# Performance work log

Measured on AMD Instinct MI355X. Metric: run time of the kernel, lower is better.

## Reference

```python
import jax, jax.numpy as jnp
import numpy as np

T, H, F, E = 1024, 2048, 4096, 8


def setup_inputs() -> dict:
    key = jax.random.key(0)
    ks = jax.random.split(key, 5)
    s = 0.02
    return {
        "x": jax.random.normal(ks[0], (1, 1, T, H), dtype=jnp.float32),
        "w_gate": jax.random.normal(ks[1], (H, E), dtype=jnp.float32) * s,
        "w1": jax.random.normal(ks[2], (E, H, F), dtype=jnp.float32) * s,
        "w3": jax.random.normal(ks[3], (E, H, F), dtype=jnp.float32) * s,
        "w2": jax.random.normal(ks[4], (E, F, H), dtype=jnp.float32) * s,
    }


def _top2_weights(logits):
    # Faithful to top_2(): emulated top-2 via max/eq/mask, then 2-way softmax
    # w0 = 1/(1+exp(ex1-ex0)) for the top-1 expert, 1-w0 for the top-2 expert.
    neg_min = jnp.finfo(logits.dtype).min
    ex0 = jnp.max(logits, axis=-1, keepdims=True)            # (1,1,T,1)
    cond0 = (logits == ex0)                                   # top-1 indicator (1,1,T,E)
    masked = jnp.where(cond0, neg_min, logits)
    ex1 = jnp.max(masked, axis=-1, keepdims=True)            # second max
    cond1 = (masked == ex1)                                   # top-2 indicator
    w0 = 1.0 / (1.0 + jnp.exp(ex1 - ex0))                    # sigmoid(ex0-ex1)
    c0 = cond0.astype(logits.dtype)
    c1 = cond1.astype(logits.dtype)
    # c0*w0 - c1*(w0-1) == c0*w0 + c1*(1-w0)
    return c0 * w0 - c1 * (w0 - 1.0)                         # (1,1,T,E)


def reference(x, w_gate, w1, w3, w2):
    # x: (1,1,T,H)
    logits = jnp.einsum("abth,he->abte", x, w_gate)          # gate (1,1,T,E)
    weights = _top2_weights(logits)                           # (1,1,T,E)
    # SwiGLU experts, all experts on all tokens (dense, as in per-device replica)
    h1 = jnp.einsum("abth,ehf->eabtf", x, w1)
    h3 = jnp.einsum("abth,ehf->eabtf", x, w3)
    y = jnp.einsum("eabtf,efh->eabth", jax.nn.silu(h1) * h3, w2)
    # per-expert scale then sum over experts (= all-gather + reduce-mask matmul)
    out = jnp.einsum("eabth,abte->abth", y, weights)
    return out
```

## Files before the change

kernel.cpp:

```cpp
#include <hip/hip_runtime.h>
#include <hip/hip_bf16.h>

#define T_DIM 1024
#define H_DIM 2048
#define F_DIM 4096
#define E_DIM 8

typedef unsigned short u16;
typedef unsigned int u32;
typedef __attribute__((ext_vector_type(8))) short bf16x8;
typedef __attribute__((ext_vector_type(4))) float f32x4;

__device__ __forceinline__ u16 f2bf(float f) {
  u32 u = __builtin_bit_cast(u32, f);
  u32 r = (u + 0x7fffu + ((u >> 16) & 1u)) >> 16;
  return (u16)r;
}

__global__ __launch_bounds__(256) void gate_cvt_kernel(
    const float* __restrict__ x, const float* __restrict__ wg,
    u16* __restrict__ xb, float* __restrict__ wts) {
  int wave = threadIdx.x >> 6;
  int lane = threadIdx.x & 63;
  int t = blockIdx.x * 4 + wave;
  const float4* x4 = reinterpret_cast<const float4*>(x) + (size_t)t * 512;
  ushort4* xb4 = reinterpret_cast<ushort4*>(xb) + (size_t)t * 512;
  const float4* wg4 = reinterpret_cast<const float4*>(wg);

  float acc[8];
#pragma unroll
  for (int e = 0; e < 8; e++) acc[e] = 0.f;

#pragma unroll
  for (int i = 0; i < 8; i++) {
    int idx = i * 64 + lane;
    float4 v = x4[idx];
    ushort4 o = {f2bf(v.x), f2bf(v.y), f2bf(v.z), f2bf(v.w)};
    xb4[idx] = o;
    float xs[4] = {v.x, v.y, v.z, v.w};
    int hbase = idx * 4;
#pragma unroll
    for (int j = 0; j < 4; j++) {
      float4 wa = wg4[(hbase + j) * 2];
      float4 wb = wg4[(hbase + j) * 2 + 1];
      acc[0] += xs[j] * wa.x; acc[1] += xs[j] * wa.y;
      acc[2] += xs[j] * wa.z; acc[3] += xs[j] * wa.w;
      acc[4] += xs[j] * wb.x; acc[5] += xs[j] * wb.y;
      acc[6] += xs[j] * wb.z; acc[7] += xs[j] * wb.w;
    }
  }
#pragma unroll
  for (int e = 0; e < 8; e++) {
#pragma unroll
    for (int off = 32; off > 0; off >>= 1) acc[e] += __shfl_xor(acc[e], off, 64);
  }
  if (lane == 0) {
    const float NEG_MIN = -3.402823466e38f;
    float ex0 = acc[0];
#pragma unroll
    for (int e = 1; e < 8; e++) ex0 = fmaxf(ex0, acc[e]);
    float masked[8];
#pragma unroll
    for (int e = 0; e < 8; e++) masked[e] = (acc[e] == ex0) ? NEG_MIN : acc[e];
    float ex1 = masked[0];
#pragma unroll
    for (int e = 1; e < 8; e++) ex1 = fmaxf(ex1, masked[e]);
    float w0 = 1.f / (1.f + expf(ex1 - ex0));
#pragma unroll
    for (int e = 0; e < 8; e++) {
      float w = (acc[e] == ex0) ? w0 : ((masked[e] == ex1) ? (1.f - w0) : 0.f);
      wts[t * 8 + e] = w;
    }
  }
}

__global__ __launch_bounds__(512) void route_kernel(
    const float* __restrict__ wts, int* __restrict__ tlist,
    int* __restrict__ counts) {
  int e = threadIdx.x >> 6;
  int lane = threadIdx.x & 63;
  int base = 0;
  for (int c = 0; c < T_DIM; c += 64) {
    float w = wts[(c + lane) * 8 + e];
    unsigned long long m = __ballot(w != 0.f);
    if (w != 0.f) {
      int pos = base + __popcll(m & ((1ull << lane) - 1ull));
      tlist[e * T_DIM + pos] = c + lane;
    }
    base += __popcll(m);
  }
  if (lane == 0) counts[e] = base;
}

__global__ __launch_bounds__(256, 2) void h_kernel(
    const u16* __restrict__ xb, const float* __restrict__ w1,
    const float* __restrict__ w3, u16* __restrict__ hout,
    const int* __restrict__ tlist, const int* __restrict__ counts) {
  int el = blockIdx.z;
  int ne = counts[el];
  int t0 = blockIdx.y * 128;
  if (t0 >= ne) return;

  __shared__ u16 As[128 * 72];
  __shared__ u16 B1s[64 * 72];
  __shared__ u16 B3s[64 * 72];
  __shared__ int toks[128];

  int f0 = blockIdx.x * 64;
  const float* b1 = w1 + (long)el * H_DIM * F_DIM;
  const float* b3 = w3 + (long)el * H_DIM * F_DIM;
  int tid = threadIdx.x;
  if (tid < 128) {
    int i = t0 + tid;
    toks[tid] = tlist[el * T_DIM + (i < ne ? i : ne - 1)];
  }
  __syncthreads();

  int wave = tid >> 6, lane = tid & 63;
  int wm = wave >> 1, wn = wave & 1;
  int mrow = lane & 15, quad = lane >> 4;

  const u16* aptr[4];
  int aoff[4];
#pragma unroll
  for (int it = 0; it < 4; it++) {
    int chunk = tid + it * 256;
    int r = chunk >> 3, c8 = (chunk & 7) << 3;
    aptr[it] = xb + (long)toks[r] * H_DIM + c8;
    aoff[it] = r * 72 + c8;
  }

  int bf4 = (tid & 15) << 2;
  int bk0 = (tid >> 4) << 2;
  int bwoff[4];
#pragma unroll
  for (int j = 0; j < 4; j++) {
    int f = bf4 + j;
    bwoff[j] = f * 72 + (bk0 ^ (((f >> 2) & 7) << 3));
  }
  const float* gb1 = b1 + (long)bk0 * F_DIM + f0 + bf4;
  const float* gb3 = b3 + (long)bk0 * F_DIM + f0 + bf4;

  int aroff[4][2], broff[2][2];
#pragma unroll
  for (int mt = 0; mt < 4; mt++)
#pragma unroll
    for (int kh = 0; kh < 2; kh++)
      aroff[mt][kh] = (wm * 64 + mt * 16 + mrow) * 72 + kh * 32 + quad * 8;
#pragma unroll
  for (int nt = 0; nt < 2; nt++) {
    int row = wn * 32 + nt * 16 + mrow;
    int sw = ((row >> 2) & 7) << 3;
#pragma unroll
    for (int kh = 0; kh < 2; kh++)
      broff[nt][kh] = row * 72 + ((kh * 32 + quad * 8) ^ sw);
  }

  f32x4 acc1[4][2], acc3[4][2];
#pragma unroll
  for (int mt = 0; mt < 4; mt++)
#pragma unroll
    for (int nt = 0; nt < 2; nt++) { acc1[mt][nt] = (f32x4)(0.f); acc3[mt][nt] = (f32x4)(0.f); }

  for (int kt = 0; kt < H_DIM; kt += 64) {
#pragma unroll
    for (int it = 0; it < 4; it++) {
      uint4 v = *reinterpret_cast<const uint4*>(aptr[it] + kt);
      *reinterpret_cast<uint4*>(&As[aoff[it]]) = v;
    }
    float4 r1[4], r3[4];
    const float* g1 = gb1 + (long)kt * F_DIM;
    const float* g3 = gb3 + (long)kt * F_DIM;
#pragma unroll
    for (int kk = 0; kk < 4; kk++) {
      r1[kk] = *reinterpret_cast<const float4*>(g1 + (long)kk * F_DIM);
      r3[kk] = *reinterpret_cast<const float4*>(g3 + (long)kk * F_DIM);
    }
#pragma unroll
    for (int j = 0; j < 4; j++) {
      u32 lo1 = (u32)f2bf(((const float*)&r1[0])[j]) | ((u32)f2bf(((const float*)&r1[1])[j]) << 16);
      u32 hi1 = (u32)f2bf(((const float*)&r1[2])[j]) | ((u32)f2bf(((const float*)&r1[3])[j]) << 16);
      u32 lo3 = (u32)f2bf(((const float*)&r3[0])[j]) | ((u32)f2bf(((const float*)&r3[1])[j]) << 16);
      u32 hi3 = (u32)f2bf(((const float*)&r3[2])[j]) | ((u32)f2bf(((const float*)&r3[3])[j]) << 16);
      uint2 p1 = {lo1, hi1}, p3 = {lo3, hi3};
      *reinterpret_cast<uint2*>(&B1s[bwoff[j]]) = p1;
      *reinterpret_cast<uint2*>(&B3s[bwoff[j]]) = p3;
    }
    __syncthreads();
#pragma unroll
    for (int kh = 0; kh < 2; kh++) {
      bf16x8 af[4], b1f[2], b3f[2];
#pragma unroll
      for (int mt = 0; mt < 4; mt++)
        af[mt] = *reinterpret_cast<const bf16x8*>(&As[aroff[mt][kh]]);
#pragma unroll
      for (int nt = 0; nt < 2; nt++) {
        b1f[nt] = *reinterpret_cast<const bf16x8*>(&B1s[broff[nt][kh]]);
        b3f[nt] = *reinterpret_cast<const bf16x8*>(&B3s[broff[nt][kh]]);
      }
#pragma unroll
      for (int mt = 0; mt < 4; mt++)
#pragma unroll
        for (int nt = 0; nt < 2; nt++) {
          acc1[mt][nt] = __builtin_amdgcn_mfma_f32_16x16x32_bf16(af[mt], b1f[nt], acc1[mt][nt], 0, 0, 0);
          acc3[mt][nt] = __builtin_amdgcn_mfma_f32_16x16x32_bf16(af[mt], b3f[nt], acc3[mt][nt], 0, 0, 0);
        }
    }
    __syncthreads();
  }
  u16* hp = hout + (long)el * T_DIM * F_DIM;
#pragma unroll
  for (int mt = 0; mt < 4; mt++) {
#pragma unroll
    for (int r = 0; r < 4; r++) {
      int row = t0 + wm * 64 + mt * 16 + quad * 4 + r;
      if (row < ne) {
#pragma unroll
        for (int nt = 0; nt < 2; nt++) {
          int col = f0 + wn * 32 + nt * 16 + mrow;
          float v1 = acc1[mt][nt][r];
          float v3 = acc3[mt][nt][r];
          float sw = (v1 / (1.f + expf(-v1))) * v3;
          hp[(long)row * F_DIM + col] = f2bf(sw);
        }
      }
    }
  }
}

__global__ __launch_bounds__(256, 2) void y_kernel(
    const u16* __restrict__ h, const float* __restrict__ w2,
    const float* __restrict__ wts, float* __restrict__ out,
    const int* __restrict__ tlist, const int* __restrict__ counts) {
  int el = blockIdx.z;
  int ne = counts[el];
  int t0 = blockIdx.y * 128;
  if (t0 >= ne) return;

  __shared__ u16 As[128 * 72];
  __shared__ u16 Bs[64 * 72];
  int n0 = blockIdx.x * 64;
  const u16* a = h + (long)el * T_DIM * F_DIM;
  const float* b = w2 + (long)el * F_DIM * H_DIM;
  int tid = threadIdx.x;
  int wave = tid >> 6, lane = tid & 63;
  int wm = wave >> 1, wn = wave & 1;
  int mrow = lane & 15, quad = lane >> 4;

  int bh4 = (tid & 15) << 2;
  int bk0 = (tid >> 4) << 2;
  int bwoff[4];
#pragma unroll
  for (int j = 0; j < 4; j++) {
    int f = bh4 + j;
    bwoff[j] = f * 72 + (bk0 ^ (((f >> 2) & 7) << 3));
  }
  const float* gb = b + (long)bk0 * H_DIM + n0 + bh4;

  int aroff[4][2], broff[2][2];
#pragma unroll
  for (int mt = 0; mt < 4; mt++)
#pragma unroll
    for (int kh = 0; kh < 2; kh++)
      aroff[mt][kh] = (wm * 64 + mt * 16 + mrow) * 72 + kh * 32 + quad * 8;
#pragma unroll
  for (int nt = 0; nt < 2; nt++) {
    int row = wn * 32 + nt * 16 + mrow;
    int sw = ((row >> 2) & 7) << 3;
#pragma unroll
    for (int kh = 0; kh < 2; kh++)
      broff[nt][kh] = row * 72 + ((kh * 32 + quad * 8) ^ sw);
  }

  f32x4 acc[4][2];
#pragma unroll
  for (int mt = 0; mt < 4; mt++)
#pragma unroll
    for (int nt = 0; nt < 2; nt++) acc[mt][nt] = (f32x4)(0.f);

  for (int kt = 0; kt < F_DIM; kt += 64) {
#pragma unroll
    for (int it = 0; it < 4; it++) {
      int chunk = tid + it * 256;
      int r = chunk >> 3, c8 = (chunk & 7) << 3;
      uint4 v = *reinterpret_cast<const uint4*>(a + (long)(t0 + r) * F_DIM + kt + c8);
      *reinterpret_cast<uint4*>(&As[r * 72 + c8]) = v;
    }
    float4 rb[4];
    const float* g = gb + (long)kt * H_DIM;
#pragma unroll
    for (int kk = 0; kk < 4; kk++)
      rb[kk] = *reinterpret_cast<const float4*>(g + (long)kk * H_DIM);
#pragma unroll
    for (int j = 0; j < 4; j++) {
      u32 lo = (u32)f2bf(((const float*)&rb[0])[j]) | ((u32)f2bf(((const float*)&rb[1])[j]) << 16);
      u32 hi = (u32)f2bf(((const float*)&rb[2])[j]) | ((u32)f2bf(((const float*)&rb[3])[j]) << 16);
      uint2 pb = {lo, hi};
      *reinterpret_cast<uint2*>(&Bs[bwoff[j]]) = pb;
    }
    __syncthreads();
#pragma unroll
    for (int kh = 0; kh < 2; kh++) {
      bf16x8 af[4], bf[2];
#pragma unroll
      for (int mt = 0; mt < 4; mt++)
        af[mt] = *reinterpret_cast<const bf16x8*>(&As[aroff[mt][kh]]);
#pragma unroll
      for (int nt = 0; nt < 2; nt++)
        bf[nt] = *reinterpret_cast<const bf16x8*>(&Bs[broff[nt][kh]]);
#pragma unroll
      for (int mt = 0; mt < 4; mt++)
#pragma unroll
        for (int nt = 0; nt < 2; nt++)
          acc[mt][nt] = __builtin_amdgcn_mfma_f32_16x16x32_bf16(af[mt], bf[nt], acc[mt][nt], 0, 0, 0);
    }
    __syncthreads();
  }
#pragma unroll
  for (int mt = 0; mt < 4; mt++) {
#pragma unroll
    for (int r = 0; r < 4; r++) {
      int row = t0 + wm * 64 + mt * 16 + quad * 4 + r;
      if (row < ne) {
        int tok = tlist[el * T_DIM + row];
        float wt = wts[tok * 8 + el];
#pragma unroll
        for (int nt = 0; nt < 2; nt++) {
          int col = n0 + wn * 32 + nt * 16 + mrow;
          unsafeAtomicAdd(&out[(long)tok * H_DIM + col], acc[mt][nt][r] * wt);
        }
      }
    }
  }
}

extern "C" void kernel_launch(void* const* d_in, const int* in_sizes, int n_in,
                              void* d_out, int out_size, void* d_ws, size_t ws_size,
                              hipStream_t stream) {
  const float* x  = (const float*)d_in[0];
  const float* wg = (const float*)d_in[1];
  const float* w1 = (const float*)d_in[2];
  const float* w3 = (const float*)d_in[3];
  const float* w2 = (const float*)d_in[4];
  float* out = (float*)d_out;

  char* p = (char*)d_ws;
  u16* xb = (u16*)p;            p += (size_t)T_DIM * H_DIM * 2;
  float* wts = (float*)p;       p += (size_t)T_DIM * E_DIM * 4;
  int* tlist = (int*)p;         p += (size_t)E_DIM * T_DIM * 4;
  int* counts = (int*)p;        p += 256;
  u16* hbuf = (u16*)p;

  gate_cvt_kernel<<<T_DIM / 4, 256, 0, stream>>>(x, wg, xb, wts);
  route_kernel<<<1, 512, 0, stream>>>(wts, tlist, counts);
  hipMemsetAsync(d_out, 0, (size_t)out_size * 4, stream);

  h_kernel<<<dim3(F_DIM / 64, T_DIM / 128, E_DIM), 256, 0, stream>>>(
      xb, w1, w3, hbuf, tlist, counts);
  y_kernel<<<dim3(H_DIM / 64, T_DIM / 128, E_DIM), 256, 0, stream>>>(
      hbuf, w2, wts, out, tlist, counts);
}
```

Baseline: 900.9 us.

## Double-buffer activation tiles via direct global-to-LDS loads and prefetch weights

Both expert GEMM kernels now load the bf16 activation tile straight into a double-buffered LDS array with global_load_lds. The next K-tile's activations and fp32 weights are prefetched while the current tile is computed, with manual waitcnt and barriers in place of __syncthreads. The A tile drops its padded layout for an XOR swizzle, and launch bounds ask for 3 blocks per CU. The goal is to hide global-load latency behind the MFMA work. The cost is more LDS and register pressure, and the hand-written vmcnt/lgkmcnt sync is fragile.

```diff
diff --git a/kernel.cpp b/kernel.cpp
--- a/kernel.cpp
+++ b/kernel.cpp
@@ -15,6 +15,18 @@
   u32 u = __builtin_bit_cast(u32, f);
   u32 r = (u + 0x7fffu + ((u >> 16) & 1u)) >> 16;
   return (u16)r;
+}
+
+__device__ __forceinline__ void gld_lds16(const void* g, void* l) {
+  __builtin_amdgcn_global_load_lds(
+      (const __attribute__((address_space(1))) u32*)g,
+      (__attribute__((address_space(3))) u32*)l, 16, 0, 0);
+}
+
+__device__ __forceinline__ void wg_barrier() {
+  asm volatile("" ::: "memory");
+  __builtin_amdgcn_s_barrier();
+  asm volatile("" ::: "memory");
 }
 
 __global__ __launch_bounds__(256) void gate_cvt_kernel(
@@ -92,7 +104,7 @@
   if (lane == 0) counts[e] = base;
 }
 
-__global__ __launch_bounds__(256, 2) void h_kernel(
+__global__ __launch_bounds__(256, 3) void h_kernel(
     const u16* __restrict__ xb, const float* __restrict__ w1,
     const float* __restrict__ w3, u16* __restrict__ hout,
     const int* __restrict__ tlist, const int* __restrict__ counts) {
@@ -101,7 +113,7 @@
   int t0 = blockIdx.y * 128;
   if (t0 >= ne) return;
 
-  __shared__ u16 As[128 * 72];
+  __shared__ u16 As[2][128 * 64];
   __shared__ u16 B1s[64 * 72];
   __shared__ u16 B3s[64 * 72];
   __shared__ int toks[128];
@@ -120,14 +132,14 @@
   int wm = wave >> 1, wn = wave & 1;
   int mrow = lane & 15, quad = lane >> 4;
 
-  const u16* aptr[4];
-  int aoff[4];
+  const u16* asrc[4];
+  int abase[4];
 #pragma unroll
   for (int it = 0; it < 4; it++) {
     int chunk = tid + it * 256;
     int r = chunk >> 3, c8 = (chunk & 7) << 3;
-    aptr[it] = xb + (long)toks[r] * H_DIM + c8;
-    aoff[it] = r * 72 + c8;
+    asrc[it] = xb + (long)toks[r] * H_DIM + (c8 ^ ((r & 7) << 3));
+    abase[it] = (it * 256 + wave * 64) * 8;
   }
 
   int bf4 = (tid & 15) << 2;
@@ -143,10 +155,12 @@
 
   int aroff[4][2], broff[2][2];
 #pragma unroll
-  for (int mt = 0; mt < 4; mt++)
+  for (int mt = 0; mt < 4; mt++) {
+    int row = wm * 64 + mt * 16 + mrow;
 #pragma unroll
     for (int kh = 0; kh < 2; kh++)
-      aroff[mt][kh] = (wm * 64 + mt * 16 + mrow) * 72 + kh * 32 + quad * 8;
+      aroff[mt][kh] = row * 64 + ((kh * 32 + quad * 8) ^ ((row & 7) << 3));
+  }
 #pragma unroll
   for (int nt = 0; nt < 2; nt++) {
     int row = wn * 32 + nt * 16 + mrow;
@@ -162,20 +176,20 @@
 #pragma unroll
     for (int nt = 0; nt < 2; nt++) { acc1[mt][nt] = (f32x4)(0.f); acc3[mt][nt] = (f32x4)(0.f); }
 
-  for (int kt = 0; kt < H_DIM; kt += 64) {
-#pragma unroll
-    for (int it = 0; it < 4; it++) {
-      uint4 v = *reinterpret_cast<const uint4*>(aptr[it] + kt);
-      *reinterpret_cast<uint4*>(&As[aoff[it]]) = v;
-    }
-    float4 r1[4], r3[4];
-    const float* g1 = gb1 + (long)kt * F_DIM;
-    const float* g3 = gb3 + (long)kt * F_DIM;
-#pragma unroll
-    for (int kk = 0; kk < 4; kk++) {
-      r1[kk] = *reinterpret_cast<const float4*>(g1 + (long)kk * F_DIM);
-      r3[kk] = *reinterpret_cast<const float4*>(g3 + (long)kk * F_DIM);
-    }
+#pragma unroll
+  for (int it = 0; it < 4; it++) gld_lds16(asrc[it], &As[0][abase[it]]);
+  float4 r1[4], r3[4];
+#pragma unroll
+  for (int kk = 0; kk < 4; kk++) {
+    r1[kk] = *reinterpret_cast<const float4*>(gb1 + (long)kk * F_DIM);
+    r3[kk] = *reinterpret_cast<const float4*>(gb3 + (long)kk * F_DIM);
+  }
+
+  const int NT = H_DIM / 64;
+#pragma unroll 2
+  for (int i = 0; i < NT; i++) {
+    int cur = i & 1;
+    asm volatile("s_waitcnt vmcnt(0)" ::: "memory");
 #pragma unroll
     for (int j = 0; j < 4; j++) {
       u32 lo1 = (u32)f2bf(((const float*)&r1[0])[j]) | ((u32)f2bf(((const float*)&r1[1])[j]) << 16);
@@ -186,13 +200,25 @@
       *reinterpret_cast<uint2*>(&B1s[bwoff[j]]) = p1;
       *reinterpret_cast<uint2*>(&B3s[bwoff[j]]) = p3;
     }
-    __syncthreads();
+    if (i + 1 < NT) {
+      long ko = (long)(i + 1) * 64;
+#pragma unroll
+      for (int it = 0; it < 4; it++) gld_lds16(asrc[it] + ko, &As[cur ^ 1][abase[it]]);
+      long kf = ko * F_DIM;
+#pragma unroll
+      for (int kk = 0; kk < 4; kk++) {
+        r1[kk] = *reinterpret_cast<const float4*>(gb1 + kf + (long)kk * F_DIM);
+        r3[kk] = *reinterpret_cast<const float4*>(gb3 + kf + (long)kk * F_DIM);
+      }
+    }
+    asm volatile("s_waitcnt lgkmcnt(0)" ::: "memory");
+    wg_barrier();
 #pragma unroll
     for (int kh = 0; kh < 2; kh++) {
       bf16x8 af[4], b1f[2], b3f[2];
 #pragma unroll
       for (int mt = 0; mt < 4; mt++)
-        af[mt] = *reinterpret_cast<const bf16x8*>(&As[aroff[mt][kh]]);
+        af[mt] = *reinterpret_cast<const bf16x8*>(&As[cur][aroff[mt][kh]]);
 #pragma unroll
       for (int nt = 0; nt < 2; nt++) {
         b1f[nt] = *reinterpret_cast<const bf16x8*>(&B1s[broff[nt][kh]]);
@@ -206,7 +232,7 @@
           acc3[mt][nt] = __builtin_amdgcn_mfma_f32_16x16x32_bf16(af[mt], b3f[nt], acc3[mt][nt], 0, 0, 0);
         }
     }
-    __syncthreads();
+    wg_barrier();
   }
   u16* hp = hout + (long)el * T_DIM * F_DIM;
 #pragma unroll
@@ -228,7 +254,7 @@
   }
 }
 
-__global__ __launch_bounds__(256, 2) void y_kernel(
+__global__ __launch_bounds__(256, 3) void y_kernel(
     const u16* __restrict__ h, const float* __restrict__ w2,
     const float* __restrict__ wts, float* __restrict__ out,
     const int* __restrict__ tlist, const int* __restrict__ counts) {
@@ -237,7 +263,7 @@
   int t0 = blockIdx.y * 128;
   if (t0 >= ne) return;
 
-  __shared__ u16 As[128 * 72];
+  __shared__ u16 As[2][128 * 64];
   __shared__ u16 Bs[64 * 72];
   int n0 = blockIdx.x * 64;
   const u16* a = h + (long)el * T_DIM * F_DIM;
@@ -247,6 +273,16 @@
   int wm = wave >> 1, wn = wave & 1;
   int mrow = lane & 15, quad = lane >> 4;
 
+  const u16* asrc[4];
+  int abase[4];
+#pragma unroll
+  for (int it = 0; it < 4; it++) {
+    int chunk = tid + it * 256;
+    int r = chunk >> 3, c8 = (chunk & 7) << 3;
+    asrc[it] = a + (long)(t0 + r) * F_DIM + (c8 ^ ((r & 7) << 3));
+    abase[it] = (it * 256 + wave * 64) * 8;
+  }
+
   int bh4 = (tid & 15) << 2;
   int bk0 = (tid >> 4) << 2;
   int bwoff[4];
@@ -259,10 +295,12 @@
 
   int aroff[4][2], broff[2][2];
 #pragma unroll
-  for (int mt = 0; mt < 4; mt++)
+  for (int mt = 0; mt < 4; mt++) {
+    int row = wm * 64 + mt * 16 + mrow;
 #pragma unroll
     for (int kh = 0; kh < 2; kh++)
-      aroff[mt][kh] = (wm * 64 + mt * 16 + mrow) * 72 + kh * 32 + quad * 8;
+      aroff[mt][kh] = row * 64 + ((kh * 32 + quad * 8) ^ ((row & 7) << 3));
+  }
 #pragma unroll
   for (int nt = 0; nt < 2; nt++) {
     int row = wn * 32 + nt * 16 + mrow;
@@ -278,19 +316,18 @@
 #pragma unroll
     for (int nt = 0; nt < 2; nt++) acc[mt][nt] = (f32x4)(0.f);
 
-  for (int kt = 0; kt < F_DIM; kt += 64) {
-#pragma unroll
-    for (int it = 0; it < 4; it++) {
-      int chunk = tid + it * 256;
-      int r = chunk >> 3, c8 = (chunk & 7) << 3;
-      uint4 v = *reinterpret_cast<const uint4*>(a + (long)(t0 + r) * F_DIM + kt + c8);
-      *reinterpret_cast<uint4*>(&As[r * 72 + c8]) = v;
-    }
-    float4 rb[4];
-    const float* g = gb + (long)kt * H_DIM;
-#pragma unroll
-    for (int kk = 0; kk < 4; kk++)
-      rb[kk] = *reinterpret_cast<const float4*>(g + (long)kk * H_DIM);
+#pragma unroll
+  for (int it = 0; it < 4; it++) gld_lds16(asrc[it], &As[0][abase[it]]);
+  float4 rb[4];
+#pragma unroll
+  for (int kk = 0; kk < 4; kk++)
+    rb[kk] = *reinterpret_cast<const float4*>(gb + (long)kk * H_DIM);
+
+  const int NT = F_DIM / 64;
+#pragma unroll 2
+  for (int i = 0; i < NT; i++) {
+    int cur = i & 1;
+    asm volatile("s_waitcnt vmcnt(0)" ::: "memory");
 #pragma unroll
     for (int j = 0; j < 4; j++) {
       u32 lo = (u32)f2bf(((const float*)&rb[0])[j]) | ((u32)f2bf(((const float*)&rb[1])[j]) << 16);
@@ -298,13 +335,23 @@
       uint2 pb = {lo, hi};
       *reinterpret_cast<uint2*>(&Bs[bwoff[j]]) = pb;
     }
-    __syncthreads();
+    if (i + 1 < NT) {
+      long ko = (long)(i + 1) * 64;
+#pragma unroll
+      for (int it = 0; it < 4; it++) gld_lds16(asrc[it] + ko, &As[cur ^ 1][abase[it]]);
+      long kf = ko * H_DIM;
+#pragma unroll
+      for (int kk = 0; kk < 4; kk++)
+        rb[kk] = *reinterpret_cast<const float4*>(gb + kf + (long)kk * H_DIM);
+    }
+    asm volatile("s_waitcnt lgkmcnt(0)" ::: "memory");
+    wg_barrier();
 #pragma unroll
     for (int kh = 0; kh < 2; kh++) {
       bf16x8 af[4], bf[2];
 #pragma unroll
       for (int mt = 0; mt < 4; mt++)
-        af[mt] = *reinterpret_cast<const bf16x8*>(&As[aroff[mt][kh]]);
+        af[mt] = *reinterpret_cast<const bf16x8*>(&As[cur][aroff[mt][kh]]);
 #pragma unroll
       for (int nt = 0; nt < 2; nt++)
         bf[nt] = *reinterpret_cast<const bf16x8*>(&Bs[broff[nt][kh]]);
@@ -314,7 +361,7 @@
         for (int nt = 0; nt < 2; nt++)
           acc[mt][nt] = __builtin_amdgcn_mfma_f32_16x16x32_bf16(af[mt], bf[nt], acc[mt][nt], 0, 0, 0);
     }
-    __syncthreads();
+    wg_barrier();
   }
 #pragma unroll
   for (int mt = 0; mt < 4; mt++) {
```

After: 822.3 us. -8.7%, faster.
